# Optimization experiments

Measured on AMD Instinct MI355X. Metric: run time of the kernel, lower is better.

## Reference

```python
import jax, jax.numpy as jnp
import numpy as np

NUM_GROUPS = 32
EPS = 1e-5


def group_norm(x, gamma, beta):
    # x: (b, c, h, w)
    b, c, h, w = x.shape
    xg = x.reshape(b, NUM_GROUPS, c // NUM_GROUPS, h, w)
    mean = xg.mean(axis=(2, 3, 4), keepdims=True)
    var = xg.var(axis=(2, 3, 4), keepdims=True)
    xn = ((xg - mean) * jax.lax.rsqrt(var + EPS)).reshape(b, c, h, w)
    return xn * gamma[None, :, None, None] + beta[None, :, None, None]


def conv1x1(x, w, b):
    # 1x1 conv == channel matmul: x (b,c,h,w), w (out,in), b (out,)
    return jnp.einsum('bchw,oc->bohw', x, w) + b[None, :, None, None]


def setup_inputs() -> dict:
    key = jax.random.key(0)
    ks = jax.random.split(key, 10)
    C = 512
    x = jax.random.normal(ks[0], (16, C, 32, 32), dtype=jnp.float32)
    s = 1.0 / np.sqrt(C)
    return {
        'x': x,
        'norm_w': jnp.ones((C,), jnp.float32),
        'norm_b': jnp.zeros((C,), jnp.float32),
        'q_w': jax.random.normal(ks[1], (C, C), jnp.float32) * s,
        'q_b': jax.random.normal(ks[2], (C,), jnp.float32) * 0.01,
        'k_w': jax.random.normal(ks[3], (C, C), jnp.float32) * s,
        'k_b': jax.random.normal(ks[4], (C,), jnp.float32) * 0.01,
        'v_w': jax.random.normal(ks[5], (C, C), jnp.float32) * s,
        'v_b': jax.random.normal(ks[6], (C,), jnp.float32) * 0.01,
        'proj_w': jax.random.normal(ks[7], (C, C), jnp.float32) * s,
        'proj_b': jax.random.normal(ks[8], (C,), jnp.float32) * 0.01,
    }


def reference(x, norm_w, norm_b, q_w, q_b, k_w, k_b, v_w, v_b, proj_w, proj_b):
    b, c, h, w = x.shape
    hn = group_norm(x, norm_w, norm_b)
    q = conv1x1(hn, q_w, q_b).reshape(b, c, h * w)  # (b, c, n)
    k = conv1x1(hn, k_w, k_b).reshape(b, c, h * w)
    v = conv1x1(hn, v_w, v_b).reshape(b, c, h * w)
    scale = jnp.float32(c) ** -0.5
    # scores[b, i, j] = sum_c q[b,c,i] * k[b,c,j]
    scores = jnp.einsum('bci,bcj->bij', q, k) * scale  # (b, n, n)
    attn = jax.nn.softmax(scores, axis=-1)
    # h_[b, c, i] = sum_j v[b,c,j] * attn[b,i,j]
    out = jnp.einsum('bcj,bij->bci', v, attn).reshape(b, c, h, w)
    return x + conv1x1(out, proj_w, proj_b)
```

## Files before the change

kernel.cpp:

```cpp
#include <hip/hip_runtime.h>

#define B_ 16
#define C_ 512
#define N_ 1024

typedef __attribute__((ext_vector_type(8))) short bf16x8_t;
typedef __attribute__((ext_vector_type(4))) float f32x4_t;

__device__ __forceinline__ unsigned short f2bf(float f) {
  unsigned int u = __float_as_uint(f);
  u += 0x7fffu + ((u >> 16) & 1u);
  return (unsigned short)(u >> 16);
}

__device__ __forceinline__ f32x4_t mfma16(bf16x8_t a, bf16x8_t b, f32x4_t c) {
  return __builtin_amdgcn_mfma_f32_16x16x32_bf16(a, b, c, 0, 0, 0);
}

__device__ __forceinline__ void gload_lds16(const void* g, void* l) {
  __builtin_amdgcn_global_load_lds(
      (const __attribute__((address_space(1))) unsigned int*)g,
      (__attribute__((address_space(3))) unsigned int*)l, 16, 0, 0);
}

__global__ __launch_bounds__(256) void castw_k(
    const float* __restrict__ qw, const float* __restrict__ kw,
    const float* __restrict__ vw, const float* __restrict__ pw,
    unsigned short* __restrict__ Wqkv, unsigned short* __restrict__ Wp) {
  int i = blockIdx.x * 256 + threadIdx.x;
  Wqkv[i] = f2bf(qw[i]);
  Wqkv[262144 + i] = f2bf(kw[i]);
  Wqkv[524288 + i] = f2bf(vw[i]);
  Wp[i] = f2bf(pw[i]);
}

__global__ __launch_bounds__(512, 1) void gn_fused_k(
    const float* __restrict__ x, const float* __restrict__ gw,
    const float* __restrict__ gb, unsigned short* __restrict__ hn) {
  int blk = blockIdx.x;
  int b = blk >> 4, gp = blk & 15;
  int t = threadIdx.x, lane = t & 63, wave = t >> 6;
  __shared__ float xs[32768];
  __shared__ float red[2][2][8];
  const float* xg = x + ((long)b * C_ + gp * 32) * N_;
  float s0 = 0.f, s20 = 0.f, s1 = 0.f, s21 = 0.f;
#pragma unroll
  for (int i = 0; i < 16; ++i) {
    int f4 = t + 512 * i;
    float4 v = ((const float4*)xg)[f4];
    float sum = v.x + v.y + v.z + v.w;
    float sq = v.x * v.x + v.y * v.y + v.z * v.z + v.w * v.w;
    if (i < 8) { s0 += sum; s20 += sq; } else { s1 += sum; s21 += sq; }
    int fi = f4 << 2;
    int c = fi >> 10, n = fi & 1023;
    int nx = n ^ (((c >> 3) & 3) << 4);
    *(float4*)&xs[(c << 10) + nx] = v;
  }
#pragma unroll
  for (int m = 1; m < 64; m <<= 1) {
    s0 += __shfl_xor(s0, m); s20 += __shfl_xor(s20, m);
    s1 += __shfl_xor(s1, m); s21 += __shfl_xor(s21, m);
  }
  if (lane == 0) {
    red[0][0][wave] = s0; red[1][0][wave] = s20;
    red[0][1][wave] = s1; red[1][1][wave] = s21;
  }
  __syncthreads();
  float m0 = 0.f, v0 = 0.f, m1 = 0.f, v1 = 0.f;
#pragma unroll
  for (int w = 0; w < 8; ++w) {
    m0 += red[0][0][w]; v0 += red[1][0][w];
    m1 += red[0][1][w]; v1 += red[1][1][w];
  }
  m0 *= (1.f / 16384.f); m1 *= (1.f / 16384.f);
  float rv0 = rsqrtf(v0 * (1.f / 16384.f) - m0 * m0 + 1e-5f);
  float rv1 = rsqrtf(v1 * (1.f / 16384.f) - m1 * m1 + 1e-5f);
  int q = t & 3;
  float mean = (q >> 1) ? m1 : m0, rv = (q >> 1) ? rv1 : rv0;
  float ga[8], be[8];
#pragma unroll
  for (int jj = 0; jj < 8; ++jj) {
    int gc = gp * 32 + q * 8 + jj;
    ga[jj] = gw[gc] * rv;
    be[jj] = gb[gc] - mean * ga[jj];
  }
  unsigned short* ob = hn + (long)b * N_ * C_ + gp * 32 + q * 8;
  int n0 = t >> 2;
  for (int it = 0; it < 8; ++it) {
    int n = n0 + (it << 7);
    int nsw = n ^ (q << 4);
    unsigned short us[8];
#pragma unroll
    for (int jj = 0; jj < 8; ++jj) {
      int c = q * 8 + jj;
      us[jj] = f2bf(xs[(c << 10) + nsw] * ga[jj] + be[jj]);
    }
    *(uint4*)(ob + (long)n * C_) = *(uint4*)us;
  }
}

__global__ __launch_bounds__(256) void gemm_qkv(
    const unsigned short* __restrict__ W, const unsigned short* __restrict__ HN,
    const float* __restrict__ qb, const float* __restrict__ kb,
    const float* __restrict__ vb, unsigned short* __restrict__ Q2,
    unsigned short* __restrict__ K2, unsigned short* __restrict__ V2,
    float scale) {
  int flat = blockIdx.x + 12 * (blockIdx.y + 8 * blockIdx.z);
  int nf = (flat & 7) * 192 + (flat >> 3);
  int bxi = nf % 12, rem = nf / 12;
  int byi = rem & 7, bz = rem >> 3;
  const unsigned short* Ab = W + (long)bxi * 128 * 512;
  const unsigned short* Bb = HN + (long)bz * N_ * C_ + (long)byi * 128 * 512;
  __shared__ char lds[32768];
  char* As = lds;
  char* Bs = lds + 16384;
  int tid = threadIdx.x;
  int lane = tid & 63, wave = tid >> 6;
  int wr = wave >> 1, wc = wave & 1;
  int lrow = lane & 15, kgrp = lane >> 4;
  f32x4_t acc[4][4];
#pragma unroll
  for (int i = 0; i < 4; ++i)
#pragma unroll
    for (int j = 0; j < 4; ++j) acc[i][j] = (f32x4_t){0.f, 0.f, 0.f, 0.f};

  int perm = (((lane & 7) ^ (lane >> 3)) << 3);
  const unsigned short* Asrc = Ab + (long)(wave * 32 + (lane >> 3)) * 512 + perm;
  const unsigned short* Bsrc = Bb + (long)(wave * 32 + (lane >> 3)) * 512 + perm;
  char* Adst = As + wave * 32 * 128;
  char* Bdst = Bs + wave * 32 * 128;

  for (int kt = 0; kt < 8; ++kt) {
    __syncthreads();
#pragma unroll
    for (int i = 0; i < 4; ++i) {
      gload_lds16(Asrc + (long)i * 8 * 512 + kt * 64, Adst + i * 1024);
      gload_lds16(Bsrc + (long)i * 8 * 512 + kt * 64, Bdst + i * 1024);
    }
    __syncthreads();
#pragma unroll
    for (int ks = 0; ks < 2; ++ks) {
      bf16x8_t af[4], bfv[4];
#pragma unroll
      for (int mi = 0; mi < 4; ++mi) {
        int r = wr * 64 + mi * 16 + lrow;
        int o = r * 128 + ks * 64 + kgrp * 16;
        o ^= (r & 7) << 4;
        af[mi] = *(bf16x8_t*)(As + o);
      }
#pragma unroll
      for (int ni = 0; ni < 4; ++ni) {
        int r = wc * 64 + ni * 16 + lrow;
        int o = r * 128 + ks * 64 + kgrp * 16;
        o ^= (r & 7) << 4;
        bfv[ni] = *(bf16x8_t*)(Bs + o);
      }
#pragma unroll
      for (int mi = 0; mi < 4; ++mi)
#pragma unroll
        for (int ni = 0; ni < 4; ++ni)
          acc[mi][ni] = mfma16(af[mi], bfv[ni], acc[mi][ni]);
    }
  }

  int slab = bxi >> 2;
  const float* bias = slab == 0 ? qb : (slab == 1 ? kb : vb);
  float scl = slab == 0 ? scale : 1.f;
  int rowloc = (bxi & 3) * 128 + wr * 64;
  int colbase = byi * 128 + wc * 64;
  unsigned short* ob =
      (slab == 0 ? Q2 : (slab == 1 ? K2 : V2)) + ((long)bz << 19);
#pragma unroll
  for (int mi = 0; mi < 4; ++mi) {
#pragma unroll
    for (int ni = 0; ni < 4; ++ni) {
      int row0 = rowloc + mi * 16 + kgrp * 4;
      int col = colbase + ni * 16 + lrow;
      unsigned short us[4];
#pragma unroll
      for (int rg = 0; rg < 4; ++rg)
        us[rg] = f2bf((acc[mi][ni][rg] + bias[row0 + rg]) * scl);
      if (slab < 2) {
        long off = ((long)(col >> 4) << 13) + ((long)(row0 >> 3) << 7) +
                   ((col & 15) << 3) + (row0 & 7);
        *(ushort4*)(ob + off) = make_ushort4(us[0], us[1], us[2], us[3]);
      } else {
        long base16 = ((long)(row0 >> 4) << 14) + ((long)(col >> 3) << 7) +
                      (col & 7) + (row0 & 15) * 8;
#pragma unroll
        for (int rg = 0; rg < 4; ++rg) ob[base16 + rg * 8] = us[rg];
      }
    }
  }
}

__global__ __launch_bounds__(512, 1) void attn_pv_k(
    const unsigned short* __restrict__ q2, const unsigned short* __restrict__ k2,
    const unsigned short* __restrict__ v2, unsigned short* __restrict__ ao) {
  int f = blockIdx.x;
  int b = f & 15, ib = f >> 4;
  int tid = threadIdx.x, lane = tid & 63, wave = tid >> 6;
  int lrow = lane & 15, kgrp = lane >> 4;
  __shared__ unsigned short P2[65536];
  __shared__ float red1[8][64];
  __shared__ float invr[64];
  {
    const unsigned short* qsrc =
        q2 + ((long)b << 19) + ((long)(ib * 4) << 13) + wave * 4096 + lane * 8;
    char* qdst = (char*)P2 + wave * 8192;
#pragma unroll
    for (int i = 0; i < 8; ++i) gload_lds16(qsrc + i * 512, qdst + i * 1024);
  }
  asm volatile("s_waitcnt vmcnt(0)" ::: "memory");
  __syncthreads();
  f32x4_t acc[4][8];
#pragma unroll
  for (int h = 0; h < 4; ++h)
#pragma unroll
    for (int t = 0; t < 8; ++t) acc[h][t] = (f32x4_t){0.f, 0.f, 0.f, 0.f};
  const unsigned short* kb =
      k2 + ((long)b << 19) + ((long)(wave * 8) << 13) + lane * 8;
  for (int ks = 0; ks < 16; ++ks) {
    bf16x8_t kf[8];
#pragma unroll
    for (int t = 0; t < 8; ++t)
      kf[t] = *(const bf16x8_t*)(kb + t * 8192 + ks * 512);
    bf16x8_t qa[4];
#pragma unroll
    for (int h = 0; h < 4; ++h)
      qa[h] = *(const bf16x8_t*)&P2[h * 8192 + ks * 512 + lane * 8];
    __builtin_amdgcn_s_setprio(1);
#pragma unroll
    for (int h = 0; h < 4; ++h)
#pragma unroll
      for (int t = 0; t < 8; ++t) acc[h][t] = mfma16(kf[t], qa[h], acc[h][t]);
    __builtin_amdgcn_s_setprio(0);
  }
  __syncthreads();
  float sm[4] = {0.f, 0.f, 0.f, 0.f};
#pragma unroll
  for (int h = 0; h < 4; ++h) {
#pragma unroll
    for (int t = 0; t < 8; ++t) {
      int jb = wave * 16 + t * 2 + (kgrp >> 1);
      int off = h * 16384 + jb * 128 + (((lrow ^ (jb & 7)) << 3) | ((kgrp & 1) << 2));
      unsigned short us[4];
#pragma unroll
      for (int rg = 0; rg < 4; ++rg) {
        float p = exp2f(acc[h][t][rg]);
        sm[h] += p;
        us[rg] = f2bf(p);
      }
      *(ushort4*)&P2[off] = make_ushort4(us[0], us[1], us[2], us[3]);
    }
  }
#pragma unroll
  for (int m = 16; m < 64; m <<= 1)
#pragma unroll
    for (int h = 0; h < 4; ++h) sm[h] += __shfl_xor(sm[h], m);
  if (kgrp == 0) {
#pragma unroll
    for (int h = 0; h < 4; ++h) red1[wave][h * 16 + lrow] = sm[h];
  }
  __syncthreads();
  if (tid < 64) {
    float s = red1[0][tid];
#pragma unroll
    for (int w = 1; w < 8; ++w) s += red1[w][tid];
    invr[tid] = 1.f / s;
  }
  __syncthreads();
  f32x4_t o[4][4];
#pragma unroll
  for (int h = 0; h < 4; ++h)
#pragma unroll
    for (int cf = 0; cf < 4; ++cf) o[h][cf] = (f32x4_t){0.f, 0.f, 0.f, 0.f};
  const char* vb2 =
      (const char*)(v2 + ((long)b << 19) + ((long)(wave * 4) << 14)) + lane * 16;
  bf16x8_t vc[4];
#pragma unroll
  for (int cf = 0; cf < 4; ++cf) vc[cf] = *(const bf16x8_t*)(vb2 + cf * 32768);
#pragma unroll
  for (int js = 0; js < 32; ++js) {
    bf16x8_t vn[4];
    if (js < 31) {
#pragma unroll
      for (int cf = 0; cf < 4; ++cf)
        vn[cf] = *(const bf16x8_t*)(vb2 + cf * 32768 + (js + 1) * 1024);
    }
    int jb = js * 4 + kgrp;
    int pox = ((lrow ^ (jb & 7)) << 3) + jb * 128;
    bf16x8_t pa[4];
#pragma unroll
    for (int h = 0; h < 4; ++h)
      pa[h] = *(const bf16x8_t*)&P2[h * 16384 + pox];
    __builtin_amdgcn_s_setprio(1);
#pragma unroll
    for (int h = 0; h < 4; ++h)
#pragma unroll
      for (int cf = 0; cf < 4; ++cf)
        o[h][cf] = mfma16(pa[h], vc[cf], o[h][cf]);
    __builtin_amdgcn_s_setprio(0);
    if (js < 31) {
#pragma unroll
      for (int cf = 0; cf < 4; ++cf) vc[cf] = vn[cf];
    }
  }
  float inv[4][4];
#pragma unroll
  for (int h = 0; h < 4; ++h)
#pragma unroll
    for (int rg = 0; rg < 4; ++rg)
      inv[h][rg] = invr[h * 16 + kgrp * 4 + rg];
  unsigned short* aob = ao + ((long)(b * N_ + ib * 64)) * C_;
#pragma unroll
  for (int h = 0; h < 4; ++h)
#pragma unroll
    for (int cf = 0; cf < 4; ++cf) {
      int c = wave * 64 + cf * 16 + lrow;
#pragma unroll
      for (int rg = 0; rg < 4; ++rg) {
        int i = h * 16 + kgrp * 4 + rg;
        aob[(long)i * C_ + c] = f2bf(o[h][cf][rg] * inv[h][rg]);
      }
    }
}

__global__ __launch_bounds__(256) void gemm_proj(
    const unsigned short* __restrict__ A, const unsigned short* __restrict__ Bm,
    const float* __restrict__ bias, const float* __restrict__ resid,
    float* __restrict__ outp) {
  int flat = blockIdx.x + 4 * (blockIdx.y + 8 * blockIdx.z);
  int nf = (flat & 7) * 64 + (flat >> 3);
  int bxi = nf & 3, byi = (nf >> 2) & 7, bz = nf >> 5;
  const unsigned short* Ab = A + (long)bxi * 128 * 512;
  const unsigned short* Bb = Bm + (long)bz * N_ * C_ + (long)byi * 128 * 512;
  __shared__ char lds[32768];
  char* As = lds;
  char* Bs = lds + 16384;
  int tid = threadIdx.x;
  int lane = tid & 63, wave = tid >> 6;
  int wr = wave >> 1, wc = wave & 1;
  int lrow = lane & 15, kgrp = lane >> 4;
  f32x4_t acc[4][4];
#pragma unroll
  for (int i = 0; i < 4; ++i)
#pragma unroll
    for (int j = 0; j < 4; ++j) acc[i][j] = (f32x4_t){0.f, 0.f, 0.f, 0.f};

  int perm = (((lane & 7) ^ (lane >> 3)) << 3);
  const unsigned short* Asrc = Ab + (long)(wave * 32 + (lane >> 3)) * 512 + perm;
  const unsigned short* Bsrc = Bb + (long)(wave * 32 + (lane >> 3)) * 512 + perm;
  char* Adst = As + wave * 32 * 128;
  char* Bdst = Bs + wave * 32 * 128;

  for (int kt = 0; kt < 8; ++kt) {
    __syncthreads();
#pragma unroll
    for (int i = 0; i < 4; ++i) {
      gload_lds16(Asrc + (long)i * 8 * 512 + kt * 64, Adst + i * 1024);
      gload_lds16(Bsrc + (long)i * 8 * 512 + kt * 64, Bdst + i * 1024);
    }
    __syncthreads();
#pragma unroll
    for (int ks = 0; ks < 2; ++ks) {
      bf16x8_t af[4], bfv[4];
#pragma unroll
      for (int mi = 0; mi < 4; ++mi) {
        int r = wr * 64 + mi * 16 + lrow;
        int o = r * 128 + ks * 64 + kgrp * 16;
        o ^= (r & 7) << 4;
        af[mi] = *(bf16x8_t*)(As + o);
      }
#pragma unroll
      for (int ni = 0; ni < 4; ++ni) {
        int r = wc * 64 + ni * 16 + lrow;
        int o = r * 128 + ks * 64 + kgrp * 16;
        o ^= (r & 7) << 4;
        bfv[ni] = *(bf16x8_t*)(Bs + o);
      }
#pragma unroll
      for (int mi = 0; mi < 4; ++mi)
#pragma unroll
        for (int ni = 0; ni < 4; ++ni)
          acc[mi][ni] = mfma16(af[mi], bfv[ni], acc[mi][ni]);
    }
  }

  int rowbase = bxi * 128 + wr * 64;
  int colbase = byi * 128 + wc * 64;
  float* ob = outp + (long)bz * C_ * N_;
  const float* rb = resid + (long)bz * C_ * N_;
#pragma unroll
  for (int mi = 0; mi < 4; ++mi) {
#pragma unroll
    for (int ni = 0; ni < 4; ++ni) {
      int row0 = rowbase + mi * 16 + kgrp * 4;
      int col = colbase + ni * 16 + lrow;
#pragma unroll
      for (int rg = 0; rg < 4; ++rg) {
        int r = row0 + rg;
        ob[(long)r * N_ + col] =
            acc[mi][ni][rg] + bias[r] + rb[(long)r * N_ + col];
      }
    }
  }
}

extern "C" void kernel_launch(void* const* d_in, const int* in_sizes, int n_in,
                              void* d_out, int out_size, void* d_ws,
                              size_t ws_size, hipStream_t stream) {
  (void)in_sizes; (void)n_in; (void)out_size; (void)ws_size;
  const float* x = (const float*)d_in[0];
  const float* nw = (const float*)d_in[1];
  const float* nb = (const float*)d_in[2];
  const float* qw = (const float*)d_in[3];
  const float* qbias = (const float*)d_in[4];
  const float* kw = (const float*)d_in[5];
  const float* kbias = (const float*)d_in[6];
  const float* vw = (const float*)d_in[7];
  const float* vbias = (const float*)d_in[8];
  const float* pw = (const float*)d_in[9];
  const float* pbias = (const float*)d_in[10];
  float* out = (float*)d_out;

  char* ws = (char*)d_ws;
  unsigned short* WQKV = (unsigned short*)(ws + 0);
  unsigned short* Wp = (unsigned short*)(ws + 1572864);
  unsigned short* HN = (unsigned short*)(ws + 2097152);
  unsigned short* Q2 = (unsigned short*)(ws + 18874368);
  unsigned short* K2 = (unsigned short*)(ws + 35651584);
  unsigned short* V2 = (unsigned short*)(ws + 52428800);
  unsigned short* AO = (unsigned short*)(ws + 69206016);

  castw_k<<<1024, 256, 0, stream>>>(qw, kw, vw, pw, WQKV, Wp);
  gn_fused_k<<<256, 512, 0, stream>>>(x, nw, nb, HN);

  const float scale = 0.06375871512f;
  gemm_qkv<<<dim3(12, 8, B_), 256, 0, stream>>>(WQKV, HN, qbias, kbias, vbias,
                                                Q2, K2, V2, scale);
  attn_pv_k<<<256, 512, 0, stream>>>(Q2, K2, V2, AO);
  gemm_proj<<<dim3(4, 8, B_), 256, 0, stream>>>(Wp, AO, pbias, x, out);
}
```

Baseline: 108.1 us.

## Fuse output projection into attention kernel and pre-swizzle projection weights

Removes the separate projection GEMM. Each attention block now writes its normalized 64-row output tile into LDS and multiplies it by the full 512x512 projection weight, adding bias and residual directly. This avoids the bf16 round trip of the attention output through global memory and one kernel launch. The projection weights are pre-swizzled into an MFMA-fragment layout during the cast kernel, which is also vectorized with fewer blocks. The trade-off is that every one of the 256 blocks rereads the whole weight matrix from global/L2 without LDS staging. The fused projection also has only 256 single-occupancy blocks, so there is less parallelism than the standalone GEMM had.

```diff
diff --git a/kernel.cpp b/kernel.cpp
--- a/kernel.cpp
+++ b/kernel.cpp
@@ -26,12 +26,26 @@
 __global__ __launch_bounds__(256) void castw_k(
     const float* __restrict__ qw, const float* __restrict__ kw,
     const float* __restrict__ vw, const float* __restrict__ pw,
-    unsigned short* __restrict__ Wqkv, unsigned short* __restrict__ Wp) {
-  int i = blockIdx.x * 256 + threadIdx.x;
-  Wqkv[i] = f2bf(qw[i]);
-  Wqkv[262144 + i] = f2bf(kw[i]);
-  Wqkv[524288 + i] = f2bf(vw[i]);
-  Wp[i] = f2bf(pw[i]);
+    unsigned short* __restrict__ Wqkv, unsigned short* __restrict__ Wpf) {
+  int idx = blockIdx.x * 256 + threadIdx.x;
+  int m = idx >> 6;
+  int k0 = (idx & 63) * 8;
+  long lin = (long)m * 512 + k0;
+#pragma unroll
+  for (int s = 0; s < 3; ++s) {
+    const float* src = s == 0 ? qw : (s == 1 ? kw : vw);
+    float4 a = *(const float4*)(src + lin);
+    float4 b = *(const float4*)(src + lin + 4);
+    unsigned short us[8] = {f2bf(a.x), f2bf(a.y), f2bf(a.z), f2bf(a.w),
+                            f2bf(b.x), f2bf(b.y), f2bf(b.z), f2bf(b.w)};
+    *(uint4*)(Wqkv + s * 262144 + lin) = *(uint4*)us;
+  }
+  float4 d = *(const float4*)(pw + lin);
+  float4 d2 = *(const float4*)(pw + lin + 4);
+  unsigned short up[8] = {f2bf(d.x),  f2bf(d.y),  f2bf(d.z),  f2bf(d.w),
+                          f2bf(d2.x), f2bf(d2.y), f2bf(d2.z), f2bf(d2.w)};
+  long fp = ((long)(m >> 4) << 13) + ((k0 >> 3) << 7) + ((m & 15) << 3);
+  *(uint4*)(Wpf + fp) = *(uint4*)up;
 }
 
 __global__ __launch_bounds__(512, 1) void gn_fused_k(
@@ -194,9 +208,11 @@
   }
 }
 
-__global__ __launch_bounds__(512, 1) void attn_pv_k(
+__global__ __launch_bounds__(512, 1) void attn_fused_k(
     const unsigned short* __restrict__ q2, const unsigned short* __restrict__ k2,
-    const unsigned short* __restrict__ v2, unsigned short* __restrict__ ao) {
+    const unsigned short* __restrict__ v2, const unsigned short* __restrict__ wpf,
+    const float* __restrict__ pbias, const float* __restrict__ x,
+    float* __restrict__ out) {
   int f = blockIdx.x;
   int b = f & 15, ib = f >> 4;
   int tid = threadIdx.x, lane = tid & 63, wave = tid >> 6;
@@ -306,102 +322,55 @@
       for (int cf = 0; cf < 4; ++cf) vc[cf] = vn[cf];
     }
   }
-  float inv[4][4];
-#pragma unroll
-  for (int h = 0; h < 4; ++h)
-#pragma unroll
-    for (int rg = 0; rg < 4; ++rg)
-      inv[h][rg] = invr[h * 16 + kgrp * 4 + rg];
-  unsigned short* aob = ao + ((long)(b * N_ + ib * 64)) * C_;
-#pragma unroll
-  for (int h = 0; h < 4; ++h)
+  __syncthreads();
+#pragma unroll
+  for (int h = 0; h < 4; ++h) {
 #pragma unroll
     for (int cf = 0; cf < 4; ++cf) {
       int c = wave * 64 + cf * 16 + lrow;
+      int cb = (c >> 3) * 128 + (c & 7);
 #pragma unroll
       for (int rg = 0; rg < 4; ++rg) {
-        int i = h * 16 + kgrp * 4 + rg;
-        aob[(long)i * C_ + c] = f2bf(o[h][cf][rg] * inv[h][rg]);
-      }
-    }
-}
-
-__global__ __launch_bounds__(256) void gemm_proj(
-    const unsigned short* __restrict__ A, const unsigned short* __restrict__ Bm,
-    const float* __restrict__ bias, const float* __restrict__ resid,
-    float* __restrict__ outp) {
-  int flat = blockIdx.x + 4 * (blockIdx.y + 8 * blockIdx.z);
-  int nf = (flat & 7) * 64 + (flat >> 3);
-  int bxi = nf & 3, byi = (nf >> 2) & 7, bz = nf >> 5;
-  const unsigned short* Ab = A + (long)bxi * 128 * 512;
-  const unsigned short* Bb = Bm + (long)bz * N_ * C_ + (long)byi * 128 * 512;
-  __shared__ char lds[32768];
-  char* As = lds;
-  char* Bs = lds + 16384;
-  int tid = threadIdx.x;
-  int lane = tid & 63, wave = tid >> 6;
-  int wr = wave >> 1, wc = wave & 1;
-  int lrow = lane & 15, kgrp = lane >> 4;
-  f32x4_t acc[4][4];
-#pragma unroll
-  for (int i = 0; i < 4; ++i)
-#pragma unroll
-    for (int j = 0; j < 4; ++j) acc[i][j] = (f32x4_t){0.f, 0.f, 0.f, 0.f};
-
-  int perm = (((lane & 7) ^ (lane >> 3)) << 3);
-  const unsigned short* Asrc = Ab + (long)(wave * 32 + (lane >> 3)) * 512 + perm;
-  const unsigned short* Bsrc = Bb + (long)(wave * 32 + (lane >> 3)) * 512 + perm;
-  char* Adst = As + wave * 32 * 128;
-  char* Bdst = Bs + wave * 32 * 128;
-
-  for (int kt = 0; kt < 8; ++kt) {
-    __syncthreads();
-#pragma unroll
-    for (int i = 0; i < 4; ++i) {
-      gload_lds16(Asrc + (long)i * 8 * 512 + kt * 64, Adst + i * 1024);
-      gload_lds16(Bsrc + (long)i * 8 * 512 + kt * 64, Bdst + i * 1024);
-    }
-    __syncthreads();
-#pragma unroll
-    for (int ks = 0; ks < 2; ++ks) {
-      bf16x8_t af[4], bfv[4];
-#pragma unroll
-      for (int mi = 0; mi < 4; ++mi) {
-        int r = wr * 64 + mi * 16 + lrow;
-        int o = r * 128 + ks * 64 + kgrp * 16;
-        o ^= (r & 7) << 4;
-        af[mi] = *(bf16x8_t*)(As + o);
-      }
-#pragma unroll
-      for (int ni = 0; ni < 4; ++ni) {
-        int r = wc * 64 + ni * 16 + lrow;
-        int o = r * 128 + ks * 64 + kgrp * 16;
-        o ^= (r & 7) << 4;
-        bfv[ni] = *(bf16x8_t*)(Bs + o);
-      }
-#pragma unroll
-      for (int mi = 0; mi < 4; ++mi)
-#pragma unroll
-        for (int ni = 0; ni < 4; ++ni)
-          acc[mi][ni] = mfma16(af[mi], bfv[ni], acc[mi][ni]);
-    }
-  }
-
-  int rowbase = bxi * 128 + wr * 64;
-  int colbase = byi * 128 + wc * 64;
-  float* ob = outp + (long)bz * C_ * N_;
-  const float* rb = resid + (long)bz * C_ * N_;
+        float inv = invr[h * 16 + kgrp * 4 + rg];
+        P2[h * 8192 + cb + ((kgrp * 4 + rg) << 3)] =
+            f2bf(o[h][cf][rg] * inv);
+      }
+    }
+  }
+  __syncthreads();
+  f32x4_t pacc[4][4];
+#pragma unroll
+  for (int mi = 0; mi < 4; ++mi)
+#pragma unroll
+    for (int ni = 0; ni < 4; ++ni) pacc[mi][ni] = (f32x4_t){0.f, 0.f, 0.f, 0.f};
+  const unsigned short* wpb = wpf + (long)wave * 32768 + lane * 8;
+  for (int ks = 0; ks < 16; ++ks) {
+    bf16x8_t af[4], bfv[4];
+#pragma unroll
+    for (int mi = 0; mi < 4; ++mi)
+      af[mi] = *(const bf16x8_t*)(wpb + mi * 8192 + ks * 512);
+#pragma unroll
+    for (int ni = 0; ni < 4; ++ni)
+      bfv[ni] = *(const bf16x8_t*)&P2[ni * 8192 + ks * 512 + lane * 8];
+    __builtin_amdgcn_s_setprio(1);
+#pragma unroll
+    for (int mi = 0; mi < 4; ++mi)
+#pragma unroll
+      for (int ni = 0; ni < 4; ++ni)
+        pacc[mi][ni] = mfma16(af[mi], bfv[ni], pacc[mi][ni]);
+    __builtin_amdgcn_s_setprio(0);
+  }
+  float* ob = out + (long)b * C_ * N_ + ib * 64;
+  const float* xb = x + (long)b * C_ * N_ + ib * 64;
 #pragma unroll
   for (int mi = 0; mi < 4; ++mi) {
 #pragma unroll
     for (int ni = 0; ni < 4; ++ni) {
-      int row0 = rowbase + mi * 16 + kgrp * 4;
-      int col = colbase + ni * 16 + lrow;
+      int n = ni * 16 + lrow;
 #pragma unroll
       for (int rg = 0; rg < 4; ++rg) {
-        int r = row0 + rg;
-        ob[(long)r * N_ + col] =
-            acc[mi][ni][rg] + bias[r] + rb[(long)r * N_ + col];
+        int c = wave * 64 + mi * 16 + kgrp * 4 + rg;
+        ob[(long)c * N_ + n] = pacc[mi][ni][rg] + pbias[c] + xb[(long)c * N_ + n];
       }
     }
   }
@@ -426,19 +395,17 @@
 
   char* ws = (char*)d_ws;
   unsigned short* WQKV = (unsigned short*)(ws + 0);
-  unsigned short* Wp = (unsigned short*)(ws + 1572864);
+  unsigned short* Wpf = (unsigned short*)(ws + 1572864);
   unsigned short* HN = (unsigned short*)(ws + 2097152);
   unsigned short* Q2 = (unsigned short*)(ws + 18874368);
   unsigned short* K2 = (unsigned short*)(ws + 35651584);
   unsigned short* V2 = (unsigned short*)(ws + 52428800);
-  unsigned short* AO = (unsigned short*)(ws + 69206016);
-
-  castw_k<<<1024, 256, 0, stream>>>(qw, kw, vw, pw, WQKV, Wp);
+
+  castw_k<<<128, 256, 0, stream>>>(qw, kw, vw, pw, WQKV, Wpf);
   gn_fused_k<<<256, 512, 0, stream>>>(x, nw, nb, HN);
 
   const float scale = 0.06375871512f;
   gemm_qkv<<<dim3(12, 8, B_), 256, 0, stream>>>(WQKV, HN, qbias, kbias, vbias,
                                                 Q2, K2, V2, scale);
-  attn_pv_k<<<256, 512, 0, stream>>>(Q2, K2, V2, AO);
-  gemm_proj<<<dim3(4, 8, B_), 256, 0, stream>>>(Wp, AO, pbias, x, out);
-}
+  attn_fused_k<<<256, 512, 0, stream>>>(Q2, K2, V2, Wpf, pbias, x, out);
+}
```

Result: faster. 102.1 us (-5.5%).
